# Performance work log

Measured on AMD Instinct MI355X. Metric: run time of the kernel, lower is better.

Reference implementation:

```python
import jax, jax.numpy as jnp
import numpy as np
import math

DIM = 2048
NUM_HEADS = 16
HEAD_DIM = DIM // NUM_HEADS
SEQ = 2048
BATCH = 4
THETA = 10000.0


def _rope_tables(seq_len, d, theta):
    # faithful to RotaryEmbedding: emb = cat([freqs, freqs], -1), then [..., ::2]
    inv_freq = 1.0 / theta ** (np.arange(0, d, 2, dtype=np.float32) / d)  # [d/2]
    t = np.arange(seq_len, dtype=np.float32)
    freqs = np.einsum('i,j->ij', t, inv_freq)          # [S, d/2]
    emb = np.concatenate([freqs, freqs], axis=-1)       # [S, d]
    cos_split = np.cos(emb)[:, ::2]                     # [S, d/2]
    sin_split = np.sin(emb)[:, ::2]                     # [S, d/2]
    return jnp.asarray(cos_split), jnp.asarray(sin_split)


def _apply_rope(x, cos_s, sin_s):
    # x: [b, h, s, d]; cos_s/sin_s: [s, d/2]
    x1 = x[..., ::2]
    x2 = x[..., 1::2]
    c = cos_s[None, None]
    s = sin_s[None, None]
    return jnp.concatenate([x1 * c - x2 * s, x1 * s + x2 * c], axis=-1)


def setup_inputs() -> dict:
    key = jax.random.key(0)
    k1, k2, k3 = jax.random.split(key, 3)
    x = jax.random.normal(k1, (BATCH, SEQ, DIM), dtype=jnp.float32)
    # causal additive mask [1,1,S,S]
    neg = jnp.finfo(jnp.float32).min
    causal = jnp.tril(jnp.ones((SEQ, SEQ), dtype=bool))
    mask = jnp.where(causal, 0.0, neg)[None, None].astype(jnp.float32)
    w_qkv = jax.random.normal(k2, (3 * DIM, DIM), dtype=jnp.float32) * (1.0 / math.sqrt(DIM))
    w_out = jax.random.normal(k3, (DIM, DIM), dtype=jnp.float32) * (1.0 / math.sqrt(DIM))
    return {"x": x, "mask": mask, "w_qkv": w_qkv, "w_out": w_out}


def reference(x, mask, w_qkv, w_out):
    b, s, _ = x.shape
    h, d = NUM_HEADS, HEAD_DIM
    qkv = jnp.einsum('bse,fe->bsf', x, w_qkv)           # [b, s, 3*dim]
    q, k, v = jnp.split(qkv, 3, axis=-1)
    # b s (h d) -> b h s d
    reshp = lambda t: t.reshape(b, s, h, d).transpose(0, 2, 1, 3)
    q, k, v = reshp(q), reshp(k), reshp(v)
    cos_s, sin_s = _rope_tables(s, d, THETA)
    q = _apply_rope(q, cos_s, sin_s)
    k = _apply_rope(k, cos_s, sin_s)
    att = jnp.einsum('bhqd,bhkd->bhqk', q, k) / math.sqrt(d)
    att = att + mask
    att = jax.nn.softmax(att, axis=-1)
    y = jnp.einsum('bhqk,bhkd->bhqd', att, v)           # [b, h, s, d]
    y = y.transpose(0, 2, 1, 3).reshape(b, s, h * d)
    return jnp.einsum('bse,fe->bsf', y, w_out)
```

## Files before the change

kernel.cpp:

```cpp
#include <hip/hip_runtime.h>

typedef unsigned short u16;
typedef unsigned int u32;
typedef __attribute__((ext_vector_type(4))) float f32x4;
typedef __attribute__((ext_vector_type(16))) float f32x16;
typedef __attribute__((ext_vector_type(8))) short bf16x8;
typedef __attribute__((ext_vector_type(4))) float float4v;
typedef __attribute__((ext_vector_type(4))) unsigned short u16x4;
typedef __attribute__((ext_vector_type(8))) unsigned short u16x8;

__device__ __forceinline__ float bf2f(u16 u) { return __uint_as_float(((u32)u) << 16); }
__device__ __forceinline__ u16 f2bf(float f) {
  u32 x = __float_as_uint(f);
  x += 0x7fffu + ((x >> 16) & 1u);
  return (u16)(x >> 16);
}
__device__ __forceinline__ u32 cvtpk(float lo, float hi_) {
  u32 r;
  asm("v_cvt_pk_bf16_f32 %0, %1, %2" : "=v"(r) : "v"(lo), "v"(hi_));
  return r;
}

__device__ __forceinline__ void gll16(const void* g, void* l) {
  __builtin_amdgcn_global_load_lds((const __attribute__((address_space(1))) void*)g,
                                   (__attribute__((address_space(3))) void*)l, 16, 0, 0);
}

#define MFMA32(a, b, c) __builtin_amdgcn_mfma_f32_32x32x16_bf16((a), (b), (c), 0, 0, 0)

#define BARRIER() __builtin_amdgcn_s_barrier()
#define LGKM0() do { asm volatile("s_waitcnt lgkmcnt(0)" ::: "memory"); \
                     __builtin_amdgcn_sched_barrier(0); } while (0)
#define VMCNT(n) do { asm volatile("s_waitcnt vmcnt(" #n ")" ::: "memory"); \
                      __builtin_amdgcn_sched_barrier(0); } while (0)

__global__ __launch_bounds__(256) void cast_kernel(const float* __restrict__ src,
                                                   u16* __restrict__ dst, int n) {
  const int stride = gridDim.x * 256 * 4;
  for (int i = (blockIdx.x * 256 + threadIdx.x) * 4; i < n; i += stride) {
    const float4v v = *(const float4v*)(src + i);
    u16x4 o;
    o[0] = f2bf(v[0]); o[1] = f2bf(v[1]); o[2] = f2bf(v[2]); o[3] = f2bf(v[3]);
    *(u16x4*)(dst + i) = o;
  }
}

__global__ __launch_bounds__(256) void rope_tables(float* __restrict__ cosd,
                                                   float* __restrict__ sind) {
  const int idx = blockIdx.x * 256 + threadIdx.x;
  const int t = idx >> 6, j = idx & 63;
  const float inv = powf(10000.0f, -(float)(j & 31) * (1.0f / 32.0f));
  const float ang = (float)t * inv;
  cosd[idx] = cosf(ang);
  sind[idx] = sinf(ang);
}

#define PH_MFMA32(MG, NG)                                                        \
  do {                                                                           \
    _Pragma("unroll") for (int i_ = 0; i_ < 2; ++i_)                             \
      _Pragma("unroll") for (int ks_ = 0; ks_ < 4; ++ks_)                        \
        acc[(MG) * 2 + i_][NG] = MFMA32(af[i_][ks_], bfr[ks_],                   \
                                        acc[(MG) * 2 + i_][NG]);                 \
  } while (0)

template <int MODE>
__global__ __launch_bounds__(512, 2) void gemm32(const u16* __restrict__ A,
                                                 const u16* __restrict__ B,
                                                 void* __restrict__ Cv, int M, int N, int K,
                                                 int lda, int ldb, int ldc) {
  __shared__ __align__(16) u16 LDS[2][2][2][128 * 64];
  const int nbn = N >> 8;
  const int nwg = gridDim.x;
  const int wg = (blockIdx.x & 7) * (nwg >> 3) + (blockIdx.x >> 3);
  const int bm = wg / nbn, bn = wg % nbn;
  const int tid = threadIdx.x;
  const int w = tid >> 6, l = tid & 63, l31 = l & 31, hi = l >> 5;
  const int wr = w >> 2, wc = w & 3;
  const u16* Abase = A + (size_t)bm * 256 * lda;
  const u16* Bbase = B + (size_t)bn * 256 * ldb;
  const int NT = K >> 6;

  f32x16 acc[4][2] = {};
  bf16x8 af[2][4], bfr[4];

  auto STAGE = [&](int sel, int h, int t) {
    const u16* src = (sel ? Bbase + (size_t)h * 128 * ldb : Abase + (size_t)h * 128 * lda) +
                     t * 64;
    const int ld = sel ? ldb : lda;
    char* dst = (char*)&LDS[t & 1][sel][h][0];
#pragma unroll
    for (int j = 0; j < 2; ++j) {
      const int o = j * 8192 + tid * 16;
      const int r = o >> 7;
      const int cb = (o & 127) ^ ((r & 7) << 4);
      gll16(src + (size_t)r * ld + (cb >> 1), dst + o);
    }
  };
  auto LDA_ = [&](int bb, int mg) {
    const char* base = (const char*)&LDS[bb][0][mg][0];
#pragma unroll
    for (int i = 0; i < 2; ++i) {
      const int R = i * 64 + wr * 32 + l31;
#pragma unroll
      for (int ks = 0; ks < 4; ++ks)
        af[i][ks] = *(const bf16x8*)(base + R * 128 + ((ks * 32 + hi * 16) ^ ((R & 7) << 4)));
    }
  };
  auto LDB_ = [&](int bb, int ng) {
    const char* base = (const char*)&LDS[bb][1][ng][0];
    const int Rb = wc * 32 + l31;
#pragma unroll
    for (int ks = 0; ks < 4; ++ks)
      bfr[ks] = *(const bf16x8*)(base + Rb * 128 + ((ks * 32 + hi * 16) ^ ((Rb & 7) << 4)));
  };

  STAGE(0, 0, 0); STAGE(1, 0, 0); STAGE(0, 1, 0); STAGE(1, 1, 0);
  if (NT > 1) { STAGE(1, 0, 1); STAGE(0, 1, 1); STAGE(1, 1, 1); }
  VMCNT(6);
  BARRIER();

  for (int T = 0; T < NT; ++T) {
    const int bb = T & 1;
    LDA_(bb, 0); LDB_(bb, 0);
    if (T + 1 < NT) STAGE(0, 0, T + 1);
    BARRIER(); LGKM0();
    __builtin_amdgcn_s_setprio(1); PH_MFMA32(0, 0); __builtin_amdgcn_s_setprio(0);
    BARRIER();
    LDA_(bb, 1);
    if (T + 2 < NT) STAGE(1, 0, T + 2);
    BARRIER(); LGKM0();
    __builtin_amdgcn_s_setprio(1); PH_MFMA32(1, 0); __builtin_amdgcn_s_setprio(0);
    BARRIER();
    LDB_(bb, 1);
    if (T + 2 < NT) STAGE(0, 1, T + 2);
    BARRIER(); LGKM0();
    __builtin_amdgcn_s_setprio(1); PH_MFMA32(1, 1); __builtin_amdgcn_s_setprio(0);
    BARRIER();
    LDA_(bb, 0);
    if (T + 2 < NT) STAGE(1, 1, T + 2);
    BARRIER(); LGKM0();
    __builtin_amdgcn_s_setprio(1); PH_MFMA32(0, 1); __builtin_amdgcn_s_setprio(0);
    if (T + 2 < NT) { VMCNT(6); } else { VMCNT(0); }
    BARRIER();
  }

#pragma unroll
  for (int fi = 0; fi < 4; ++fi) {
    const int mg = fi >> 1, i = fi & 1;
    const int row0 = bm * 256 + mg * 128 + i * 64 + wr * 32;
#pragma unroll
    for (int ng = 0; ng < 2; ++ng) {
      const int col = bn * 256 + ng * 128 + wc * 32 + l31;
      const f32x16 a = acc[mg * 2 + i][ng];
      if (MODE == 0) {
        float* C = (float*)Cv;
#pragma unroll
        for (int r = 0; r < 16; ++r)
          C[(size_t)(row0 + (r & 3) + 8 * (r >> 2) + 4 * hi) * ldc + col] = a[r];
      } else if (bn < 16) {
        u16* C = (u16*)Cv;
#pragma unroll
        for (int r = 0; r < 16; ++r)
          C[(size_t)(row0 + (r & 3) + 8 * (r >> 2) + 4 * hi) * 6144 + col] = f2bf(a[r]);
      } else {
        u16* C = (u16*)Cv;
        const int batch = row0 >> 11;
        const int srow0 = row0 & 2047;
        const int vcol = col - 4096;
        u16* vbase = C + (size_t)((batch * 16 + (vcol >> 7)) * 128 + (vcol & 127)) * 6144 +
                     4096 + srow0 + 4 * hi;
#pragma unroll
        for (int q_ = 0; q_ < 4; ++q_) {
          union { u32 u[2]; u16x4 v; } pk;
          pk.u[0] = cvtpk(a[4 * q_ + 0], a[4 * q_ + 1]);
          pk.u[1] = cvtpk(a[4 * q_ + 2], a[4 * q_ + 3]);
          *(u16x4*)(vbase + 8 * q_) = pk.v;
        }
      }
    }
  }
}

__global__ __launch_bounds__(256) void rope_apply_inplace(u16* __restrict__ qkvb,
                                                          const float* __restrict__ cosd,
                                                          const float* __restrict__ sind) {
  const int wid = blockIdx.x * 4 + (threadIdx.x >> 6);
  const int j = threadIdx.x & 63;
  const int h = wid & 15;
  const int m = wid >> 4;
  const int s = m & 2047;
  const float c = cosd[s * 64 + j];
  const float sn = sind[s * 64 + j];
  u16* qp = qkvb + (size_t)m * 6144 + h * 128;
  u16* kp = qp + 2048;
  const u32 qv = *(const u32*)(qp + 2 * j);
  const u32 kv = *(const u32*)(kp + 2 * j);
  const float q1 = bf2f((u16)(qv & 0xffff)), q2 = bf2f((u16)(qv >> 16));
  const float k1 = bf2f((u16)(kv & 0xffff)), k2 = bf2f((u16)(kv >> 16));
  qp[j]      = f2bf(q1 * c - q2 * sn);
  qp[64 + j] = f2bf(q1 * sn + q2 * c);
  kp[j]      = f2bf(k1 * c - k2 * sn);
  kp[64 + j] = f2bf(k1 * sn + k2 * c);
}

__global__ __launch_bounds__(512, 2) void flash_attn(u16* __restrict__ qkvb) {
  __shared__ __align__(16) char smem[65536];
  const int bh = blockIdx.x;
  const int qt = 7 - blockIdx.y;
  const int b = bh >> 4, h = bh & 15;
  const int tid = threadIdx.x;
  const int w = tid >> 6, l = tid & 63;
  const int l31 = l & 31, hi = l >> 5;

  const int q0 = qt * 256 + w * 32;
  const int qg = q0 + l31;

  bf16x8 qf[8];
  {
    const u16* Qrow = qkvb + (size_t)(b * 2048 + qg) * 6144 + h * 128 + hi * 8;
#pragma unroll
    for (int d = 0; d < 8; ++d) qf[d] = *(const bf16x8*)(Qrow + d * 16);
  }

  f32x16 ot[4];
#pragma unroll
  for (int dt = 0; dt < 4; ++dt) ot[dt] = 0.f;
  float mrun = -1e30f, lrun = 0.f;

  const int NT = 4 * qt + 4;
  const u16* Kg0 = qkvb + (size_t)b * 2048 * 6144 + 2048 + h * 128;
  const u16* Vg0 = qkvb + (size_t)bh * 128 * 6144 + 4096;

  auto STAGE = [&](int t) {
    const u16* Kg = Kg0 + (size_t)t * 64 * 6144;
    const u16* Vg = Vg0 + t * 64;
    char* kd = smem + (t & 1) * 16384;
    char* vd = smem + 32768 + (t & 1) * 16384;
#pragma unroll
    for (int j = 0; j < 2; ++j) {
      const int o = j * 8192 + tid * 16;
      {
        const int r = o >> 8;
        const int cb = (o & 255) ^ ((r & 15) << 4);
        gll16(Kg + (size_t)r * 6144 + (cb >> 1), kd + o);
      }
      {
        const int r = o >> 7;
        const int cb = (o & 127) ^ ((r & 7) << 4);
        gll16(Vg + (size_t)r * 6144 + (cb >> 1), vd + o);
      }
    }
  };

  STAGE(0);
  VMCNT(0);
  BARRIER();

  for (int kt = 0; kt < NT; ++kt) {
    if (kt + 1 < NT) STAGE(kt + 1);

    if (kt * 64 <= q0 + 31) {
      const char* Kb = smem + (kt & 1) * 16384;
      const char* Vb = smem + 32768 + (kt & 1) * 16384;

      f32x16 sa[2];
      sa[0] = 0.f; sa[1] = 0.f;
#pragma unroll
      for (int ks2 = 0; ks2 < 2; ++ks2) {
        const int R = ks2 * 32 + l31;
#pragma unroll
        for (int d = 0; d < 8; ++d) {
          const bf16x8 kf = *(const bf16x8*)(Kb + R * 256 +
                                             ((d * 32 + hi * 16) ^ ((R & 15) << 4)));
          sa[ks2] = MFMA32(kf, qf[d], sa[ks2]);
        }
      }

      const float SCALE = 0.08838834764831845f;
      float tmax = -1e30f;
      if (kt * 64 + 63 > q0) {
#pragma unroll
        for (int ks2 = 0; ks2 < 2; ++ks2)
#pragma unroll
          for (int rg = 0; rg < 16; ++rg) {
            const int key = kt * 64 + ks2 * 32 + (rg & 3) + 8 * (rg >> 2) + 4 * hi;
            float sv = sa[ks2][rg] * SCALE;
            sv = (key > qg) ? -1e30f : sv;
            sa[ks2][rg] = sv;
            tmax = fmaxf(tmax, sv);
          }
      } else {
#pragma unroll
        for (int ks2 = 0; ks2 < 2; ++ks2)
#pragma unroll
          for (int rg = 0; rg < 16; ++rg) {
            const float sv = sa[ks2][rg] * SCALE;
            sa[ks2][rg] = sv;
            tmax = fmaxf(tmax, sv);
          }
      }
      tmax = fmaxf(tmax, __shfl_xor(tmax, 32));

      const float mnew = fmaxf(mrun, tmax);
      const float alpha = __expf(mrun - mnew);
      mrun = mnew;
      float rsum = 0.f;
#pragma unroll
      for (int ks2 = 0; ks2 < 2; ++ks2)
#pragma unroll
        for (int rg = 0; rg < 16; ++rg) {
          const float pv = __expf(sa[ks2][rg] - mnew);
          sa[ks2][rg] = pv;
          rsum += pv;
        }
      rsum += __shfl_xor(rsum, 32);
      lrun = lrun * alpha + rsum;
#pragma unroll
      for (int dt = 0; dt < 4; ++dt)
#pragma unroll
        for (int rg = 0; rg < 16; ++rg) ot[dt][rg] *= alpha;

      bf16x8 pfrag[4];
#pragma unroll
      for (int t = 0; t < 4; ++t) {
        const int ks2 = t >> 1;
        const int gA = 2 * (t & 1);
        const int gB = gA + 1;
        const u32 a0 = cvtpk(sa[ks2][gA * 4 + 0], sa[ks2][gA * 4 + 1]);
        const u32 a1 = cvtpk(sa[ks2][gA * 4 + 2], sa[ks2][gA * 4 + 3]);
        const u32 b0 = cvtpk(sa[ks2][gB * 4 + 0], sa[ks2][gB * 4 + 1]);
        const u32 b1 = cvtpk(sa[ks2][gB * 4 + 2], sa[ks2][gB * 4 + 3]);
        const u32 snd0 = hi ? a0 : b0;
        const u32 snd1 = hi ? a1 : b1;
        const u32 rcv0 = (u32)__shfl_xor((int)snd0, 32);
        const u32 rcv1 = (u32)__shfl_xor((int)snd1, 32);
        union { u32 u[4]; bf16x8 v; } pk;
        pk.u[0] = hi ? rcv0 : a0;
        pk.u[1] = hi ? rcv1 : a1;
        pk.u[2] = hi ? b0 : rcv0;
        pk.u[3] = hi ? b1 : rcv1;
        pfrag[t] = pk.v;
      }

#pragma unroll
      for (int dt = 0; dt < 4; ++dt) {
        const int R = dt * 32 + l31;
#pragma unroll
        for (int t = 0; t < 4; ++t) {
          const bf16x8 vf = *(const bf16x8*)(Vb + R * 128 +
                                             ((t * 32 + hi * 16) ^ ((R & 7) << 4)));
          ot[dt] = MFMA32(vf, pfrag[t], ot[dt]);
        }
      }
    }

    VMCNT(0);
    BARRIER();
  }

  const float inv = 1.0f / lrun;
  char* E = smem + w * 8192;
#pragma unroll
  for (int dt = 0; dt < 4; ++dt)
#pragma unroll
    for (int rp = 0; rp < 8; ++rp) {
      const int rg = 2 * rp;
      const int d0 = dt * 32 + (rg & 3) + 8 * (rg >> 2) + 4 * hi;
      const u32 pkv = cvtpk(ot[dt][rg] * inv, ot[dt][rg + 1] * inv);
      *(u32*)(E + l31 * 256 + ((d0 * 2) ^ ((l31 & 15) << 4))) = pkv;
    }
#pragma unroll
  for (int p = 0; p < 8; ++p) {
    const int q = p * 4 + (l >> 4);
    const int c = l & 15;
    const bf16x8 vv = *(const bf16x8*)(E + q * 256 + ((c * 16) ^ ((q & 15) << 4)));
    *(bf16x8*)(qkvb + (size_t)(b * 2048 + q0 + q) * 6144 + h * 128 + c * 8) = vv;
  }
}

extern "C" void kernel_launch(void* const* d_in, const int* in_sizes, int n_in,
                              void* d_out, int out_size, void* d_ws, size_t ws_size,
                              hipStream_t stream) {
  const float* x     = (const float*)d_in[0];
  const float* w_qkv = (const float*)d_in[2];
  const float* w_out = (const float*)d_in[3];
  float* out = (float*)d_out;
  char* ws = (char*)d_ws;

  u16* woutb = (u16*)(ws);
  u16* xb    = (u16*)(ws + ((size_t)8 << 20));
  u16* wqkvb = (u16*)(ws + ((size_t)40 << 20));
  u16* qkvb  = (u16*)(ws + ((size_t)64 << 20));
  float* cosd = (float*)(ws + ((size_t)160 << 20));
  float* sind = (float*)(ws + ((size_t)160 << 20) + ((size_t)1 << 19));

  cast_kernel<<<2048, 256, 0, stream>>>(x, xb, 8192 * 2048);
  cast_kernel<<<2048, 256, 0, stream>>>(w_qkv, wqkvb, 6144 * 2048);
  cast_kernel<<<1024, 256, 0, stream>>>(w_out, woutb, 2048 * 2048);
  rope_tables<<<512, 256, 0, stream>>>(cosd, sind);
  gemm32<1><<<768, 512, 0, stream>>>(xb, wqkvb, qkvb, 8192, 6144, 2048,
                                     2048, 2048, 6144);
  rope_apply_inplace<<<32768, 256, 0, stream>>>(qkvb, cosd, sind);
  flash_attn<<<dim3(64, 8), 512, 0, stream>>>(qkvb);
  gemm32<0><<<256, 512, 0, stream>>>(qkvb, woutb, out, 8192, 2048, 2048,
                                     6144, 2048, 2048);
}
```

Before: 465.3 us.

## Switch GEMM to 16x16x32 MFMA tiles with reordered B-reuse phases

Replaces the 32x32x16 bf16 MFMA in both projection GEMMs with 16x16x32 MFMA. Each wave now holds 8x4 f32x4 accumulators and two B fragment sets, so the four-phase loop can be reordered to reuse B fragments across phases and cut LDS reads. The stage issue order and output write mapping are adjusted to match. The change adds register pressure, and the last phase has no LDS wait, so the ordering must stay correct; the V-transposed stores also become narrower.

New measurement: 416.3 us. 1.12x faster.

```diff
diff --git a/kernel.cpp b/kernel.cpp
--- a/kernel.cpp
+++ b/kernel.cpp
@@ -26,6 +26,7 @@
                                    (__attribute__((address_space(3))) void*)l, 16, 0, 0);
 }
 
+#define MFMA_BF16(a, b, c) __builtin_amdgcn_mfma_f32_16x16x32_bf16((a), (b), (c), 0, 0, 0)
 #define MFMA32(a, b, c) __builtin_amdgcn_mfma_f32_32x32x16_bf16((a), (b), (c), 0, 0, 0)
 
 #define BARRIER() __builtin_amdgcn_s_barrier()
@@ -55,33 +56,46 @@
   sind[idx] = sinf(ang);
 }
 
-#define PH_MFMA32(MG, NG)                                                        \
+#define PH_MFMA(MG, NG, BF)                                                      \
   do {                                                                           \
-    _Pragma("unroll") for (int i_ = 0; i_ < 2; ++i_)                             \
-      _Pragma("unroll") for (int ks_ = 0; ks_ < 4; ++ks_)                        \
-        acc[(MG) * 2 + i_][NG] = MFMA32(af[i_][ks_], bfr[ks_],                   \
-                                        acc[(MG) * 2 + i_][NG]);                 \
+    _Pragma("unroll") for (int i_ = 0; i_ < 4; ++i_)                             \
+      _Pragma("unroll") for (int jn_ = 0; jn_ < 2; ++jn_)                        \
+        _Pragma("unroll") for (int ks_ = 0; ks_ < 2; ++ks_)                      \
+          acc[(MG) * 4 + i_][(NG) * 2 + jn_] =                                   \
+              MFMA_BF16(af[i_][ks_], BF[jn_][ks_],                               \
+                        acc[(MG) * 4 + i_][(NG) * 2 + jn_]);                     \
   } while (0)
 
+#define LDB_M(bb, ng, BF)                                                        \
+  do {                                                                           \
+    const char* base_ = (const char*)&LDS[bb][1][ng][0];                         \
+    _Pragma("unroll") for (int jn_ = 0; jn_ < 2; ++jn_) {                        \
+      const int R_ = jn_ * 64 + wc * 16 + l15;                                   \
+      _Pragma("unroll") for (int ks_ = 0; ks_ < 2; ++ks_)                        \
+        BF[jn_][ks_] = *(const bf16x8*)(base_ + R_ * 128 +                       \
+                                        ((ks_ * 64 + l4 * 16) ^ ((R_ & 7) << 4)));\
+    }                                                                            \
+  } while (0)
+
 template <int MODE>
-__global__ __launch_bounds__(512, 2) void gemm32(const u16* __restrict__ A,
-                                                 const u16* __restrict__ B,
-                                                 void* __restrict__ Cv, int M, int N, int K,
-                                                 int lda, int ldb, int ldc) {
+__global__ __launch_bounds__(512, 2) void gemm_bt8(const u16* __restrict__ A,
+                                                   const u16* __restrict__ B,
+                                                   void* __restrict__ Cv, int M, int N, int K,
+                                                   int lda, int ldb, int ldc) {
   __shared__ __align__(16) u16 LDS[2][2][2][128 * 64];
   const int nbn = N >> 8;
   const int nwg = gridDim.x;
   const int wg = (blockIdx.x & 7) * (nwg >> 3) + (blockIdx.x >> 3);
   const int bm = wg / nbn, bn = wg % nbn;
   const int tid = threadIdx.x;
-  const int w = tid >> 6, l = tid & 63, l31 = l & 31, hi = l >> 5;
+  const int w = tid >> 6, l = tid & 63, l15 = l & 15, l4 = l >> 4;
   const int wr = w >> 2, wc = w & 3;
   const u16* Abase = A + (size_t)bm * 256 * lda;
   const u16* Bbase = B + (size_t)bn * 256 * ldb;
   const int NT = K >> 6;
 
-  f32x16 acc[4][2] = {};
-  bf16x8 af[2][4], bfr[4];
+  f32x4 acc[8][4] = {};
+  bf16x8 af[4][2], bfr0[2][2], bfr1[2][2];
 
   auto STAGE = [&](int sel, int h, int t) {
     const u16* src = (sel ? Bbase + (size_t)h * 128 * ldb : Abase + (size_t)h * 128 * lda) +
@@ -99,83 +113,72 @@
   auto LDA_ = [&](int bb, int mg) {
     const char* base = (const char*)&LDS[bb][0][mg][0];
 #pragma unroll
-    for (int i = 0; i < 2; ++i) {
-      const int R = i * 64 + wr * 32 + l31;
-#pragma unroll
-      for (int ks = 0; ks < 4; ++ks)
-        af[i][ks] = *(const bf16x8*)(base + R * 128 + ((ks * 32 + hi * 16) ^ ((R & 7) << 4)));
+    for (int i = 0; i < 4; ++i) {
+      const int R = i * 32 + wr * 16 + l15;
+#pragma unroll
+      for (int ks = 0; ks < 2; ++ks)
+        af[i][ks] = *(const bf16x8*)(base + R * 128 + ((ks * 64 + l4 * 16) ^ ((R & 7) << 4)));
     }
   };
-  auto LDB_ = [&](int bb, int ng) {
-    const char* base = (const char*)&LDS[bb][1][ng][0];
-    const int Rb = wc * 32 + l31;
-#pragma unroll
-    for (int ks = 0; ks < 4; ++ks)
-      bfr[ks] = *(const bf16x8*)(base + Rb * 128 + ((ks * 32 + hi * 16) ^ ((Rb & 7) << 4)));
-  };
 
   STAGE(0, 0, 0); STAGE(1, 0, 0); STAGE(0, 1, 0); STAGE(1, 1, 0);
-  if (NT > 1) { STAGE(1, 0, 1); STAGE(0, 1, 1); STAGE(1, 1, 1); }
+  if (NT > 1) { STAGE(1, 0, 1); STAGE(1, 1, 1); STAGE(0, 1, 1); }
   VMCNT(6);
   BARRIER();
 
   for (int T = 0; T < NT; ++T) {
     const int bb = T & 1;
-    LDA_(bb, 0); LDB_(bb, 0);
+    LDA_(bb, 0); LDB_M(bb, 0, bfr0);
     if (T + 1 < NT) STAGE(0, 0, T + 1);
     BARRIER(); LGKM0();
-    __builtin_amdgcn_s_setprio(1); PH_MFMA32(0, 0); __builtin_amdgcn_s_setprio(0);
-    BARRIER();
-    LDA_(bb, 1);
+    __builtin_amdgcn_s_setprio(1); PH_MFMA(0, 0, bfr0); __builtin_amdgcn_s_setprio(0);
+    BARRIER();
+    LDB_M(bb, 1, bfr1);
     if (T + 2 < NT) STAGE(1, 0, T + 2);
     BARRIER(); LGKM0();
-    __builtin_amdgcn_s_setprio(1); PH_MFMA32(1, 0); __builtin_amdgcn_s_setprio(0);
-    BARRIER();
-    LDB_(bb, 1);
-    if (T + 2 < NT) STAGE(0, 1, T + 2);
-    BARRIER(); LGKM0();
-    __builtin_amdgcn_s_setprio(1); PH_MFMA32(1, 1); __builtin_amdgcn_s_setprio(0);
-    BARRIER();
-    LDA_(bb, 0);
+    __builtin_amdgcn_s_setprio(1); PH_MFMA(0, 1, bfr1); __builtin_amdgcn_s_setprio(0);
+    BARRIER();
+    LDA_(bb, 1);
     if (T + 2 < NT) STAGE(1, 1, T + 2);
     BARRIER(); LGKM0();
-    __builtin_amdgcn_s_setprio(1); PH_MFMA32(0, 1); __builtin_amdgcn_s_setprio(0);
+    __builtin_amdgcn_s_setprio(1); PH_MFMA(1, 1, bfr1); __builtin_amdgcn_s_setprio(0);
+    BARRIER();
+    if (T + 2 < NT) STAGE(0, 1, T + 2);
+    BARRIER();
+    __builtin_amdgcn_s_setprio(1); PH_MFMA(1, 0, bfr0); __builtin_amdgcn_s_setprio(0);
     if (T + 2 < NT) { VMCNT(6); } else { VMCNT(0); }
     BARRIER();
   }
 
 #pragma unroll
-  for (int fi = 0; fi < 4; ++fi) {
-    const int mg = fi >> 1, i = fi & 1;
-    const int row0 = bm * 256 + mg * 128 + i * 64 + wr * 32;
-#pragma unroll
-    for (int ng = 0; ng < 2; ++ng) {
-      const int col = bn * 256 + ng * 128 + wc * 32 + l31;
-      const f32x16 a = acc[mg * 2 + i][ng];
+  for (int mf = 0; mf < 8; ++mf) {
+    const int mg = mf >> 2, i = mf & 3;
+    const int row0 = bm * 256 + mg * 128 + i * 32 + wr * 16 + l4 * 4;
+#pragma unroll
+    for (int f = 0; f < 4; ++f) {
+      const int col = bn * 256 + f * 64 + wc * 16 + l15;
+      const f32x4 a = acc[mf][f];
       if (MODE == 0) {
         float* C = (float*)Cv;
 #pragma unroll
-        for (int r = 0; r < 16; ++r)
-          C[(size_t)(row0 + (r & 3) + 8 * (r >> 2) + 4 * hi) * ldc + col] = a[r];
+        for (int r = 0; r < 4; ++r)
+          C[(size_t)(row0 + r) * ldc + col] = a[r];
       } else if (bn < 16) {
         u16* C = (u16*)Cv;
 #pragma unroll
-        for (int r = 0; r < 16; ++r)
-          C[(size_t)(row0 + (r & 3) + 8 * (r >> 2) + 4 * hi) * 6144 + col] = f2bf(a[r]);
+        for (int r = 0; r < 4; ++r)
+          C[(size_t)(row0 + r) * 6144 + col] = f2bf(a[r]);
       } else {
         u16* C = (u16*)Cv;
         const int batch = row0 >> 11;
-        const int srow0 = row0 & 2047;
+        const int s0 = row0 & 2047;
         const int vcol = col - 4096;
-        u16* vbase = C + (size_t)((batch * 16 + (vcol >> 7)) * 128 + (vcol & 127)) * 6144 +
-                     4096 + srow0 + 4 * hi;
-#pragma unroll
-        for (int q_ = 0; q_ < 4; ++q_) {
-          union { u32 u[2]; u16x4 v; } pk;
-          pk.u[0] = cvtpk(a[4 * q_ + 0], a[4 * q_ + 1]);
-          pk.u[1] = cvtpk(a[4 * q_ + 2], a[4 * q_ + 3]);
-          *(u16x4*)(vbase + 8 * q_) = pk.v;
-        }
+        u16* vb = C + (size_t)((batch * 16 + (vcol >> 7)) * 128 + (vcol & 127)) * 6144 +
+                  4096 + s0;
+        union { u32 u[2]; u16x4 v; } pk;
+        pk.u[0] = cvtpk(a[0], a[1]);
+        pk.u[1] = cvtpk(a[2], a[3]);
+        *(u16x4*)vb = pk.v;
       }
     }
   }
@@ -398,10 +401,10 @@
   cast_kernel<<<2048, 256, 0, stream>>>(w_qkv, wqkvb, 6144 * 2048);
   cast_kernel<<<1024, 256, 0, stream>>>(w_out, woutb, 2048 * 2048);
   rope_tables<<<512, 256, 0, stream>>>(cosd, sind);
-  gemm32<1><<<768, 512, 0, stream>>>(xb, wqkvb, qkvb, 8192, 6144, 2048,
-                                     2048, 2048, 6144);
+  gemm_bt8<1><<<768, 512, 0, stream>>>(xb, wqkvb, qkvb, 8192, 6144, 2048,
+                                       2048, 2048, 6144);
   rope_apply_inplace<<<32768, 256, 0, stream>>>(qkvb, cosd, sind);
   flash_attn<<<dim3(64, 8), 512, 0, stream>>>(qkvb);
-  gemm32<0><<<256, 512, 0, stream>>>(qkvb, woutb, out, 8192, 2048, 2048,
-                                     6144, 2048, 2048);
-}
+  gemm_bt8<0><<<256, 512, 0, stream>>>(qkvb, woutb, out, 8192, 2048, 2048,
+                                       6144, 2048, 2048);
+}
```
